# Performance work log

Measured on AMD Instinct MI355X. Metric: run time of the kernel, lower is better.

The kernel has to match this reference:

```python
import jax, jax.numpy as jnp
import numpy as np

TAU = 0.5
EPS = 1e-8


def setup_inputs() -> dict:
    key = jax.random.key(0)
    k1, k2, k3 = jax.random.split(key, 3)
    N, D = 100000, 128
    x_r = jax.random.normal(k1, (N, D), dtype=jnp.float32)
    x_pos = jax.random.normal(k2, (N, D), dtype=jnp.float32)
    x_neg = jax.random.normal(k3, (N, D), dtype=jnp.float32)
    return {"x_r": x_r, "x_pos": x_pos, "x_neg": x_neg}


def _diag_sim(z1, z2):
    # Only the diagonal of exp(z1 @ z2.T / (|z1||z2|.T) / tau) survives the
    # eye() mask in the original, so compute just the row-wise cosine sims.
    dot = jnp.sum(z1 * z2, axis=-1)                      # [N]
    den = jnp.linalg.norm(z1, axis=-1) * jnp.linalg.norm(z2, axis=-1)  # [N]
    return jnp.exp(dot / den / TAU)                      # [N]


def reference(x_r, x_pos, x_neg):
    pos = _diag_sim(x_r, x_pos)          # diag of pos_score
    neg = _diag_sim(x_r, x_neg)          # diag of neg_score
    ss = pos / (neg + EPS)               # [N]
    loss = -jnp.log(jnp.sum(ss))         # scalar; .mean() of scalar is identity
    return loss
```

## Files before the change

kernel.cpp:

```cpp
#include <hip/hip_runtime.h>
#include <math.h>

#define TAU_INV 2.0f
#define EPS 1e-8f

__global__ __launch_bounds__(256) void contrast_partial(
    const float* __restrict__ xr, const float* __restrict__ xp,
    const float* __restrict__ xn, float* __restrict__ partials, int N)
{
    const int lane   = threadIdx.x & 31;
    const int lgrp   = threadIdx.x >> 5;
    const int stride = gridDim.x * 8;

    float acc = 0.0f;
    for (int g = blockIdx.x * 8 + lgrp; g < N; g += stride) {
        const size_t base = (size_t)g * 128;
        const float4 r = ((const float4*)(xr + base))[lane];
        const float4 p = ((const float4*)(xp + base))[lane];
        const float4 n = ((const float4*)(xn + base))[lane];

        float s_rp = r.x*p.x + r.y*p.y + r.z*p.z + r.w*p.w;
        float s_rn = r.x*n.x + r.y*n.y + r.z*n.z + r.w*n.w;
        float s_rr = r.x*r.x + r.y*r.y + r.z*r.z + r.w*r.w;
        float s_pp = p.x*p.x + p.y*p.y + p.z*p.z + p.w*p.w;
        float s_nn = n.x*n.x + n.y*n.y + n.z*n.z + n.w*n.w;

        #pragma unroll
        for (int off = 16; off > 0; off >>= 1) {
            s_rp += __shfl_xor(s_rp, off);
            s_rn += __shfl_xor(s_rn, off);
            s_rr += __shfl_xor(s_rr, off);
            s_pp += __shfl_xor(s_pp, off);
            s_nn += __shfl_xor(s_nn, off);
        }

        const float nr  = sqrtf(s_rr);
        const float pos = expf(s_rp / (nr * sqrtf(s_pp)) * TAU_INV);
        const float neg = expf(s_rn / (nr * sqrtf(s_nn)) * TAU_INV);
        acc += pos / (neg + EPS);
    }

    __shared__ float part[8];
    if (lane == 0) part[lgrp] = acc;
    __syncthreads();
    if (threadIdx.x == 0) {
        float t = 0.0f;
        #pragma unroll
        for (int i = 0; i < 8; ++i) t += part[i];
        partials[blockIdx.x] = t;
    }
}

__global__ __launch_bounds__(1024) void contrast_final(
    const float* __restrict__ partials, float* __restrict__ out, int nblk)
{
    float s = 0.0f;
    for (int i = threadIdx.x; i < nblk; i += 1024)
        s += partials[i];

    #pragma unroll
    for (int off = 32; off > 0; off >>= 1)
        s += __shfl_xor(s, off);

    __shared__ float w[16];
    if ((threadIdx.x & 63) == 0) w[threadIdx.x >> 6] = s;
    __syncthreads();
    if (threadIdx.x == 0) {
        float t = 0.0f;
        #pragma unroll
        for (int i = 0; i < 16; ++i) t += w[i];
        out[0] = -logf(t);
    }
}

extern "C" void kernel_launch(void* const* d_in, const int* in_sizes, int n_in,
                              void* d_out, int out_size, void* d_ws, size_t ws_size,
                              hipStream_t stream) {
    const float* xr = (const float*)d_in[0];
    const float* xp = (const float*)d_in[1];
    const float* xn = (const float*)d_in[2];
    float* out      = (float*)d_out;
    float* partials = (float*)d_ws;

    const int N = in_sizes[0] / 128;

    int nblk = (N + 7) / 8;
    const int cap = (int)(ws_size / sizeof(float));
    if (nblk > cap) nblk = cap;

    contrast_partial<<<nblk, 256, 0, stream>>>(xr, xp, xn, partials, N);
    contrast_final<<<1, 1024, 0, stream>>>(partials, out, nblk);
}
```

Measured before the change: 164.1 us.

## Map each row to 8 lanes with DPP reduction and fast math

```diff
diff --git a/kernel.cpp b/kernel.cpp
--- a/kernel.cpp
+++ b/kernel.cpp
@@ -4,49 +4,59 @@
 #define TAU_INV 2.0f
 #define EPS 1e-8f
 
+template<int CTRL>
+__device__ __forceinline__ float dpp_add(float x) {
+    int y = __builtin_amdgcn_update_dpp(0, __float_as_int(x), CTRL, 0xF, 0xF, true);
+    return x + __int_as_float(y);
+}
+
 __global__ __launch_bounds__(256) void contrast_partial(
     const float* __restrict__ xr, const float* __restrict__ xp,
     const float* __restrict__ xn, float* __restrict__ partials, int N)
 {
-    const int lane   = threadIdx.x & 31;
-    const int lgrp   = threadIdx.x >> 5;
-    const int stride = gridDim.x * 8;
+    const int l8    = threadIdx.x & 7;
+    const int rgrp  = threadIdx.x >> 3;
+    const int rstep = gridDim.x * 32;
 
     float acc = 0.0f;
-    for (int g = blockIdx.x * 8 + lgrp; g < N; g += stride) {
-        const size_t base = (size_t)g * 128;
-        const float4 r = ((const float4*)(xr + base))[lane];
-        const float4 p = ((const float4*)(xp + base))[lane];
-        const float4 n = ((const float4*)(xn + base))[lane];
+    for (int row = blockIdx.x * 32 + rgrp; row < N; row += rstep) {
+        const size_t base = (size_t)row * 128;
+        const float4* r4 = (const float4*)(xr + base);
+        const float4* p4 = (const float4*)(xp + base);
+        const float4* n4 = (const float4*)(xn + base);
 
-        float s_rp = r.x*p.x + r.y*p.y + r.z*p.z + r.w*p.w;
-        float s_rn = r.x*n.x + r.y*n.y + r.z*n.z + r.w*n.w;
-        float s_rr = r.x*r.x + r.y*r.y + r.z*r.z + r.w*r.w;
-        float s_pp = p.x*p.x + p.y*p.y + p.z*p.z + p.w*p.w;
-        float s_nn = n.x*n.x + n.y*n.y + n.z*n.z + n.w*n.w;
-
+        float s_rp = 0.f, s_rn = 0.f, s_rr = 0.f, s_pp = 0.f, s_nn = 0.f;
         #pragma unroll
-        for (int off = 16; off > 0; off >>= 1) {
-            s_rp += __shfl_xor(s_rp, off);
-            s_rn += __shfl_xor(s_rn, off);
-            s_rr += __shfl_xor(s_rr, off);
-            s_pp += __shfl_xor(s_pp, off);
-            s_nn += __shfl_xor(s_nn, off);
+        for (int j = 0; j < 4; ++j) {
+            const float4 r = r4[j * 8 + l8];
+            const float4 p = p4[j * 8 + l8];
+            const float4 n = n4[j * 8 + l8];
+            s_rp += r.x*p.x + r.y*p.y + r.z*p.z + r.w*p.w;
+            s_rn += r.x*n.x + r.y*n.y + r.z*n.z + r.w*n.w;
+            s_rr += r.x*r.x + r.y*r.y + r.z*r.z + r.w*r.w;
+            s_pp += p.x*p.x + p.y*p.y + p.z*p.z + p.w*p.w;
+            s_nn += n.x*n.x + n.y*n.y + n.z*n.z + n.w*n.w;
         }
 
-        const float nr  = sqrtf(s_rr);
-        const float pos = expf(s_rp / (nr * sqrtf(s_pp)) * TAU_INV);
-        const float neg = expf(s_rn / (nr * sqrtf(s_nn)) * TAU_INV);
+        s_rp = dpp_add<0xB1>(s_rp); s_rp = dpp_add<0x4E>(s_rp); s_rp = dpp_add<0x141>(s_rp);
+        s_rn = dpp_add<0xB1>(s_rn); s_rn = dpp_add<0x4E>(s_rn); s_rn = dpp_add<0x141>(s_rn);
+        s_rr = dpp_add<0xB1>(s_rr); s_rr = dpp_add<0x4E>(s_rr); s_rr = dpp_add<0x141>(s_rr);
+        s_pp = dpp_add<0xB1>(s_pp); s_pp = dpp_add<0x4E>(s_pp); s_pp = dpp_add<0x141>(s_pp);
+        s_nn = dpp_add<0xB1>(s_nn); s_nn = dpp_add<0x4E>(s_nn); s_nn = dpp_add<0x141>(s_nn);
+
+        const float inv_r = rsqrtf(s_rr);
+        const float pos = __expf(s_rp * inv_r * rsqrtf(s_pp) * TAU_INV);
+        const float neg = __expf(s_rn * inv_r * rsqrtf(s_nn) * TAU_INV);
         acc += pos / (neg + EPS);
     }
 
-    __shared__ float part[8];
-    if (lane == 0) part[lgrp] = acc;
+    __shared__ float part[32];
+    if (l8 == 0) part[rgrp] = acc;
     __syncthreads();
     if (threadIdx.x == 0) {
-        float t = 0.0f;
+        float t = 0.f;
         #pragma unroll
-        for (int i = 0; i < 8; ++i) t += part[i];
+        for (int i = 0; i < 32; ++i) t += part[i];
         partials[blockIdx.x] = t;
     }
 }
@@ -66,7 +76,7 @@
     if ((threadIdx.x & 63) == 0) w[threadIdx.x >> 6] = s;
     __syncthreads();
     if (threadIdx.x == 0) {
-        float t = 0.0f;
+        float t = 0.f;
         #pragma unroll
         for (int i = 0; i < 16; ++i) t += w[i];
         out[0] = -logf(t);
@@ -84,7 +94,7 @@
 
     const int N = in_sizes[0] / 128;
 
-    int nblk = (N + 7) / 8;
+    int nblk = (N + 31) / 32;
     const int cap = (int)(ws_size / sizeof(float));
     if (nblk > cap) nblk = cap;
 
```

Result: no change. 164.6 us (+0.3%).
